# Kernel optimization log

Measured on AMD Instinct MI355X. Metric: run time of the kernel, lower is better.

Reference implementation:

```python
import jax, jax.numpy as jnp
import numpy as np

B, C, H, W = 8, 256, 128, 128
P = 7          # patch_size (odd)
N = 500        # n_infer (eval mode)
HIDDEN = C // 16  # reduction=16


def setup_inputs() -> dict:
    key = jax.random.key(0)
    ks = jax.random.split(key, 8)
    def s(k, shape, fan_in):
        return jax.random.normal(k, shape, jnp.float32) * (1.0 / np.sqrt(fan_in))
    return {
        "x_main": jax.random.normal(ks[0], (B, C, H, W), jnp.float32),
        "x_aux": jax.random.normal(ks[1], (B, C, H, W), jnp.float32),
        "scorer_w": s(ks[2], (C,), C),            # 1x1 conv C->1
        "scorer_b": s(ks[3], (1,), C),
        "fc1_w": s(ks[4], (3 * C, HIDDEN), 3 * C),
        "fc1_b": jnp.zeros((HIDDEN,), jnp.float32),
        "fc2_w": s(ks[5], (HIDDEN, C), HIDDEN),
        "fc2_b": jnp.zeros((C,), jnp.float32),
        "proj_w": s(ks[6], (C, C), C),
        "proj_b": jnp.zeros((C,), jnp.float32),
        "n": N,
    }


def _sample_patch_feats(feat, px, py):
    # feat: [C,H,W]; px,py: [n,p,p] pixel coords (align_corners=False convention).
    # Bilinear sample with zero padding, then pool 0.5*(mean+max) over the patch.
    c, h, w = feat.shape
    x0 = jnp.floor(px); y0 = jnp.floor(py)
    wx1 = px - x0; wy1 = py - y0
    def gather(yi, xi):
        valid = ((yi >= 0) & (yi < h) & (xi >= 0) & (xi < w)).astype(feat.dtype)
        yc = jnp.clip(yi, 0, h - 1).astype(jnp.int32)
        xc = jnp.clip(xi, 0, w - 1).astype(jnp.int32)
        return feat[:, yc, xc] * valid  # [C,n,p,p]
    patch = (gather(y0, x0) * ((1 - wy1) * (1 - wx1))
             + gather(y0, x0 + 1) * ((1 - wy1) * wx1)
             + gather(y0 + 1, x0) * (wy1 * (1 - wx1))
             + gather(y0 + 1, x0 + 1) * (wy1 * wx1))  # [C,n,p,p]
    v = 0.5 * (patch.mean(axis=(2, 3)) + patch.max(axis=(2, 3)))  # [C,n]
    return v.T  # [n,C]


def reference(x_main, x_aux, scorer_w, scorer_b, fc1_w, fc1_b, fc2_w, fc2_b, proj_w, proj_b, n):
    b, c, h, w = x_main.shape
    # saliency scores -> topk indices over flattened HW
    score = jax.nn.sigmoid(jnp.einsum('bchw,c->bhw', x_main, scorer_w) + scorer_b[0])
    score = score.reshape(b, h * w)
    _, idx = jax.lax.top_k(score, n)  # [b,n] int32
    idx_y = idx // w
    idx_x = idx - idx_y * w
    # build the (clamped) normalized grid exactly as the torch module does,
    # then convert to pixel coords: px = ((g+1)*W - 1)/2 (align_corners=False)
    r = P // 2
    d = jnp.arange(-r, r + 1, dtype=jnp.float32)
    yy, xx = jnp.meshgrid(d, d, indexing='ij')
    off_x = xx * (2.0 / w); off_y = yy * (2.0 / h)           # [p,p]
    cx = (idx_x.astype(jnp.float32) + 0.5) * (2.0 / w) - 1.0  # [b,n]
    cy = (idx_y.astype(jnp.float32) + 0.5) * (2.0 / h) - 1.0
    gx = jnp.clip(cx[:, :, None, None] + off_x, -1.0, 1.0)    # [b,n,p,p]
    gy = jnp.clip(cy[:, :, None, None] + off_y, -1.0, 1.0)
    px = ((gx + 1.0) * w - 1.0) * 0.5
    py = ((gy + 1.0) * h - 1.0) * 0.5
    sample = jax.vmap(_sample_patch_feats)
    v_main = sample(x_main, px, py)  # [b,n,C]
    v_aux = sample(x_aux, px, py)    # aux_in_proj is Identity (c_main==c_aux)
    # instance-level cross attention
    sim = jnp.einsum('bnc,bmc->bnm', v_main, v_aux) / jnp.sqrt(jnp.float32(c))
    attn = jax.nn.softmax(sim, axis=-1)
    v_hat = jnp.einsum('bnm,bmc->bnc', attn, v_aux)
    # gated fusion MLP
    z = jnp.concatenate([v_main, v_hat, v_main - v_hat], axis=-1)  # [b,n,3C]
    gate = jax.nn.sigmoid(jax.nn.relu(z @ fc1_w + fc1_b) @ fc2_w + fc2_b)
    v_fused = v_main + gate * (v_main - v_hat)
    v_inj = v_fused @ proj_w + proj_b  # [b,n,C]
    # scatter-add reinjection at the topk locations
    inject = jnp.zeros((b, h * w, c), x_main.dtype)
    inject = inject.at[jnp.arange(b)[:, None], idx].add(v_inj)
    inject = inject.reshape(b, h, w, c).transpose(0, 3, 1, 2)
    return x_main + inject
```

## Files before the change

### kernel.cpp

```cpp
#include <hip/hip_runtime.h>
#include <cstdint>
#include <cstddef>

#define HW    16384
#define CCH   256
#define WID   128
#define NB    8
#define NSEL  500
#define NPAD  512

__device__ __forceinline__ unsigned key_of(float f) {
  unsigned u = __float_as_uint(f);
  return (u & 0x80000000u) ? ~u : (u | 0x80000000u);
}

__global__ __launch_bounds__(256) void score_kernel(const float* __restrict__ x,
                                                    const float* __restrict__ w,
                                                    float* __restrict__ logits) {
  __shared__ float ws[CCH];
  int tid = threadIdx.x;
  ws[tid] = w[tid];
  __syncthreads();
  int pix = blockIdx.x * 256 + tid;
  int b = pix >> 14, p = pix & (HW - 1);
  const float* xp = x + ((size_t)b << 22) + p;
  float acc = 0.f;
#pragma unroll 16
  for (int c = 0; c < CCH; c++) acc += xp[(size_t)c * HW] * ws[c];
  logits[pix] = acc;
}

__global__ __launch_bounds__(1024) void topk_kernel(const float* __restrict__ logits,
                                                    int* __restrict__ idx_out,
                                                    int* __restrict__ map) {
  int b = blockIdx.x, tid = threadIdx.x;
  const float* lg = logits + (size_t)b * HW;
  __shared__ unsigned hist[256];
  __shared__ unsigned sscan[1024];
  __shared__ unsigned bc_prefix;
  __shared__ int bc_want;
  __shared__ int cnt;

  unsigned kreg[16];
#pragma unroll
  for (int j = 0; j < 4; j++) {
    float4 v = *(const float4*)&lg[tid * 16 + j * 4];
    kreg[4 * j + 0] = key_of(v.x);
    kreg[4 * j + 1] = key_of(v.y);
    kreg[4 * j + 2] = key_of(v.z);
    kreg[4 * j + 3] = key_of(v.w);
  }
  for (int p = tid; p < HW; p += 1024) map[(size_t)b * HW + p] = -1;

  unsigned prefix = 0;
  int want = NSEL;
  for (int shift = 24; shift >= 0; shift -= 8) {
    if (tid < 256) hist[tid] = 0;
    __syncthreads();
#pragma unroll
    for (int j = 0; j < 16; j++) {
      unsigned u = kreg[j];
      bool m = (shift == 24) || ((u >> (shift + 8)) == (prefix >> (shift + 8)));
      if (m) atomicAdd(&hist[(u >> shift) & 255u], 1u);
    }
    __syncthreads();
    unsigned h = (tid < 256) ? hist[tid] : 0u;
    if (tid < 256) sscan[tid] = h;
    __syncthreads();
    for (int o = 1; o < 256; o <<= 1) {
      unsigned v = (tid < 256 && tid + o < 256) ? sscan[tid + o] : 0u;
      __syncthreads();
      if (tid < 256) sscan[tid] += v;
      __syncthreads();
    }
    if (tid < 256) {
      unsigned above = sscan[tid] - h;
      if ((int)sscan[tid] >= want && (int)above < want) {
        bc_prefix = prefix | ((unsigned)tid << shift);
        bc_want = want - (int)above;
      }
    }
    __syncthreads();
    prefix = bc_prefix;
    want = bc_want;
    __syncthreads();
  }
  unsigned thr = prefix;

  int local = 0;
#pragma unroll
  for (int j = 0; j < 16; j++) local += (kreg[j] == thr) ? 1 : 0;
  sscan[tid] = (unsigned)local;
  if (tid == 0) cnt = 0;
  __syncthreads();
  for (int o = 1; o < 1024; o <<= 1) {
    unsigned v = (tid >= o) ? sscan[tid - o] : 0u;
    __syncthreads();
    sscan[tid] += v;
    __syncthreads();
  }
  int rank = (int)sscan[tid] - local;
#pragma unroll
  for (int j = 0; j < 16; j++) {
    unsigned u = kreg[j];
    bool take = (u > thr);
    if (u == thr) { if (rank < want) take = true; rank++; }
    if (take) {
      int s = atomicAdd(&cnt, 1);
      int p = tid * 16 + j;
      idx_out[b * NPAD + s] = p;
      map[(size_t)b * HW + p] = s;
    }
  }
}

__device__ __forceinline__ void patch_weights(int p, int* xc, int* yc, float* wx, float* wy) {
  int iy = p >> 7, ix = p & (WID - 1);
#pragma unroll
  for (int d = 0; d < 7; d++) {
    int t = ix + d - 3;
    bool in = (t >= 0) && (t < WID);
    xc[d] = in ? t : (t < 0 ? 0 : WID - 1);
    wx[d] = in ? 1.f : 0.5f;
    t = iy + d - 3;
    in = (t >= 0) && (t < WID);
    yc[d] = in ? t : (t < 0 ? 0 : WID - 1);
    wy[d] = in ? 1.f : 0.5f;
  }
}

__global__ __launch_bounds__(512) void gather_plane_kernel(const float* __restrict__ xm,
                                                           const float* __restrict__ xa,
                                                           const int* __restrict__ idx,
                                                           float* __restrict__ vmainT,
                                                           float* __restrict__ vauxT) {
  extern __shared__ float plane[];
  int c = blockIdx.x, b = blockIdx.y, z = blockIdx.z;
  int tid = threadIdx.x;
  const float* src = (z == 0 ? xm : xa) + ((size_t)(b * CCH + c)) * HW;
  float* dst = (z == 0 ? vmainT : vauxT) + (((size_t)(b * CCH + c)) << 9);
#pragma unroll
  for (int j = 0; j < 8; j++) {
    int p4 = tid + j * 512;
    *(float4*)&plane[p4 * 4] = *(const float4*)&src[p4 * 4];
  }
  __syncthreads();
  if (tid < NSEL) {
    int p = idx[b * NPAD + tid];
    float wx[7], wy[7];
    int xc[7], yc[7];
    patch_weights(p, xc, yc, wx, wy);
    float s = 0.f, mx = -INFINITY;
#pragma unroll
    for (int dy = 0; dy < 7; dy++) {
      int rb = yc[dy] * WID;
      float wyd = wy[dy];
#pragma unroll
      for (int dx = 0; dx < 7; dx++) {
        float v = plane[rb + xc[dx]] * (wyd * wx[dx]);
        s += v;
        mx = fmaxf(mx, v);
      }
    }
    dst[tid] = 0.5f * (s * (1.f / 49.f) + mx);
  }
}

template <int M, int N, int K, bool AT, bool BT, bool BSHARED, int EPI>
__global__ __launch_bounds__(256) void gemm_kernel(const float* __restrict__ A,
                                                   const float* __restrict__ B,
                                                   float* __restrict__ C,
                                                   const float* __restrict__ bias) {
  constexpr int BM = 64, BN = 64, BK = 16;
  __shared__ float As[BM][BK + 1];
  __shared__ float Bs[BK][BN + 1];
  int tid = threadIdx.x;
  int bx = blockIdx.x, by = blockIdx.y, b = blockIdx.z;
  const float* Ab = A + (size_t)b * M * K;
  const float* Bb = BSHARED ? B : (B + (size_t)b * ((size_t)K * N));
  int tx = tid & 15, ty = tid >> 4;
  float acc[4][4] = {};
  int ar = tid >> 2, ac4 = (tid & 3) * 4;
  int br = tid >> 4, bc4 = (tid & 15) * 4;

  for (int k0 = 0; k0 < K; k0 += BK) {
    if (!AT) {
      const float4 av = *(const float4*)&Ab[(size_t)(by * BM + ar) * K + k0 + ac4];
      As[ar][ac4 + 0] = av.x; As[ar][ac4 + 1] = av.y;
      As[ar][ac4 + 2] = av.z; As[ar][ac4 + 3] = av.w;
    } else {
      int kr = tid >> 4, mc = (tid & 15) * 4;
      const float4 av = *(const float4*)&Ab[(size_t)(k0 + kr) * M + by * BM + mc];
      As[mc + 0][kr] = av.x; As[mc + 1][kr] = av.y;
      As[mc + 2][kr] = av.z; As[mc + 3][kr] = av.w;
    }
    if (!BT) {
      const float4 bv = *(const float4*)&Bb[(size_t)(k0 + br) * N + bx * BN + bc4];
      Bs[br][bc4 + 0] = bv.x; Bs[br][bc4 + 1] = bv.y;
      Bs[br][bc4 + 2] = bv.z; Bs[br][bc4 + 3] = bv.w;
    } else {
      const float4 bv = *(const float4*)&Bb[(size_t)(bx * BN + ar) * K + k0 + ac4];
      Bs[ac4 + 0][ar] = bv.x; Bs[ac4 + 1][ar] = bv.y;
      Bs[ac4 + 2][ar] = bv.z; Bs[ac4 + 3][ar] = bv.w;
    }
    __syncthreads();
#pragma unroll
    for (int kk = 0; kk < BK; kk++) {
      float a[4], bb[4];
#pragma unroll
      for (int r = 0; r < 4; r++) a[r] = As[ty * 4 + r][kk];
#pragma unroll
      for (int s = 0; s < 4; s++) bb[s] = Bs[kk][tx * 4 + s];
#pragma unroll
      for (int r = 0; r < 4; r++)
#pragma unroll
        for (int s = 0; s < 4; s++) acc[r][s] += a[r] * bb[s];
    }
    __syncthreads();
  }
  if (EPI == 2) {
#pragma unroll
    for (int s = 0; s < 4; s++) {
      int col = bx * BN + tx * 4 + s;
      float bv = bias[col];
#pragma unroll
      for (int r = 0; r < 4; r++) {
        int row = by * BM + ty * 4 + r;
        C[((size_t)b * N + col) * M + row] = acc[r][s] + bv;
      }
    }
  } else {
    float scale = (EPI == 1) ? 0.0625f : 1.f;
#pragma unroll
    for (int r = 0; r < 4; r++) {
      int row = by * BM + ty * 4 + r;
#pragma unroll
      for (int s = 0; s < 4; s++) {
        int col = bx * BN + tx * 4 + s;
        C[((size_t)b * M + row) * N + col] = acc[r][s] * scale;
      }
    }
  }
}

__global__ __launch_bounds__(256) void softmax_kernel(float* __restrict__ sim) {
  int i = blockIdx.x, b = blockIdx.y, tid = threadIdx.x;
  float* row = sim + ((size_t)b * NPAD + i) * NPAD;
  float v0 = (tid < NSEL) ? row[tid] : -INFINITY;
  int j1 = tid + 256;
  float v1 = (j1 < NSEL) ? row[j1] : -INFINITY;
  float m = fmaxf(v0, v1);
  for (int o = 32; o; o >>= 1) m = fmaxf(m, __shfl_down(m, o));
  __shared__ float red[4];
  __shared__ float bm, bs;
  int wave = tid >> 6, lane = tid & 63;
  if (lane == 0) red[wave] = m;
  __syncthreads();
  if (tid == 0) bm = fmaxf(fmaxf(red[0], red[1]), fmaxf(red[2], red[3]));
  __syncthreads();
  m = bm;
  float e0 = (tid < NSEL) ? expf(v0 - m) : 0.f;
  float e1 = (j1 < NSEL) ? expf(v1 - m) : 0.f;
  float s = e0 + e1;
  for (int o = 32; o; o >>= 1) s += __shfl_down(s, o);
  if (lane == 0) red[wave] = s;
  __syncthreads();
  if (tid == 0) bs = 1.f / (red[0] + red[1] + red[2] + red[3]);
  __syncthreads();
  row[tid] = e0 * bs;
  row[j1] = e1 * bs;
}

__global__ __launch_bounds__(256) void mlp_kernel(const float* __restrict__ vmainT,
                                                  const float* __restrict__ vhat,
                                                  const float* __restrict__ fc1w,
                                                  const float* __restrict__ fc1b,
                                                  const float* __restrict__ fc2w,
                                                  const float* __restrict__ fc2b,
                                                  float* __restrict__ vfused) {
  int i = blockIdx.x, b = blockIdx.y, c = threadIdx.x;
  size_t base = ((size_t)b * NPAD + i) * CCH + c;
  float vm = vmainT[(((size_t)(b * CCH + c)) << 9) + i];
  float vh = vhat[base], vd = vm - vh;
  const float* w0 = fc1w + (size_t)c * 16;
  const float* w1 = fc1w + (size_t)(256 + c) * 16;
  const float* w2 = fc1w + (size_t)(512 + c) * 16;
  float ph[16];
#pragma unroll
  for (int k = 0; k < 16; k++) ph[k] = vm * w0[k] + vh * w1[k] + vd * w2[k];
#pragma unroll
  for (int o = 32; o; o >>= 1)
#pragma unroll
    for (int k = 0; k < 16; k++) ph[k] += __shfl_down(ph[k], o);
  __shared__ float red[4][16];
  __shared__ float hsh[16];
  int wave = c >> 6, lane = c & 63;
  if (lane == 0)
#pragma unroll
    for (int k = 0; k < 16; k++) red[wave][k] = ph[k];
  __syncthreads();
  if (c < 16) {
    float s = red[0][c] + red[1][c] + red[2][c] + red[3][c] + fc1b[c];
    hsh[c] = fmaxf(s, 0.f);
  }
  __syncthreads();
  float g = fc2b[c];
#pragma unroll
  for (int k = 0; k < 16; k++) g += hsh[k] * fc2w[k * 256 + c];
  g = 1.f / (1.f + expf(-g));
  vfused[base] = vm + g * vd;
}

__global__ __launch_bounds__(256) void final_kernel(const float* __restrict__ x,
                                                    const int* __restrict__ map,
                                                    const float* __restrict__ vinjT,
                                                    float* __restrict__ out) {
  int gid = blockIdx.x * 256 + threadIdx.x;
  int p4 = gid & 4095;
  int c = (gid >> 12) & 255;
  int b = gid >> 20;
  size_t xoff = (((size_t)(b * 256 + c)) << 14) + ((size_t)p4 << 2);
  float4 xv = *(const float4*)(x + xoff);
  const int4 mv = *(const int4*)(map + ((size_t)b << 14) + (p4 << 2));
  const float* vt = vinjT + ((size_t)(b * 256 + c) << 9);
  if (mv.x >= 0) xv.x += vt[mv.x];
  if (mv.y >= 0) xv.y += vt[mv.y];
  if (mv.z >= 0) xv.z += vt[mv.z];
  if (mv.w >= 0) xv.w += vt[mv.w];
  *(float4*)(out + xoff) = xv;
}

extern "C" void kernel_launch(void* const* d_in, const int* in_sizes, int n_in,
                              void* d_out, int out_size, void* d_ws, size_t ws_size,
                              hipStream_t stream) {
  const float* x_main   = (const float*)d_in[0];
  const float* x_aux    = (const float*)d_in[1];
  const float* scorer_w = (const float*)d_in[2];
  const float* fc1_w = (const float*)d_in[4];
  const float* fc1_b = (const float*)d_in[5];
  const float* fc2_w = (const float*)d_in[6];
  const float* fc2_b = (const float*)d_in[7];
  const float* proj_w = (const float*)d_in[8];
  const float* proj_b = (const float*)d_in[9];
  (void)in_sizes; (void)n_in; (void)out_size; (void)ws_size;

  float* ws = (float*)d_ws;
  float* logits = ws;
  int*   idx    = (int*)(ws + 131072);
  int*   map    = (int*)(ws + 135168);
  float* vmainT = ws + 266240;
  float* vauxT  = ws + 1314816;
  float* vhat   = ws + 2363392;
  float* vfused = ws + 3411968;
  float* sim    = ws + 4460544;
  float* vinjT  = vhat;
  float* out = (float*)d_out;

  score_kernel<<<512, 256, 0, stream>>>(x_main, scorer_w, logits);
  topk_kernel<<<NB, 1024, 0, stream>>>(logits, idx, map);
  gather_plane_kernel<<<dim3(CCH, NB, 2), 512, HW * sizeof(float), stream>>>(
      x_main, x_aux, idx, vmainT, vauxT);
  gemm_kernel<NPAD, NPAD, CCH, true, false, false, 1>
      <<<dim3(8, 8, NB), 256, 0, stream>>>(vmainT, vauxT, sim, nullptr);
  softmax_kernel<<<dim3(NPAD, NB), 256, 0, stream>>>(sim);
  gemm_kernel<NPAD, CCH, NPAD, false, true, false, 0>
      <<<dim3(4, 8, NB), 256, 0, stream>>>(sim, vauxT, vhat, nullptr);
  mlp_kernel<<<dim3(NPAD, NB), 256, 0, stream>>>(vmainT, vhat, fc1_w, fc1_b,
                                                 fc2_w, fc2_b, vfused);
  gemm_kernel<NPAD, CCH, CCH, false, false, true, 2>
      <<<dim3(4, 8, NB), 256, 0, stream>>>(vfused, proj_w, vinjT, proj_b);
  final_kernel<<<32768, 256, 0, stream>>>(x_main, map, vinjT, out);
}
```

Before: 540.8 us.

## Pipeline channel-plane loads in gather kernel and vectorize GEMM shared-memory reads

The gather kernel now handles 8 channels per block. It prefetches the next channel plane into registers while computing on the current plane in shared memory, and hoists index and weight setup so it runs once per block instead of once per channel. The patch reduction is also factored by rows. The GEMM stores its A tile k-major, so inner-loop reads become float4 shared-memory loads. The trade-off is fewer blocks in the gather (512 instead of 4096), higher register pressure from the 8 float4 prefetch, and it now writes zeros to the padded rows.

```diff
diff --git a/kernel.cpp b/kernel.cpp
--- a/kernel.cpp
+++ b/kernel.cpp
@@ -8,6 +8,7 @@
 #define NB    8
 #define NSEL  500
 #define NPAD  512
+#define CPG   8
 
 __device__ __forceinline__ unsigned key_of(float f) {
   unsigned u = __float_as_uint(f);
@@ -129,40 +130,64 @@
   }
 }
 
-__global__ __launch_bounds__(512) void gather_plane_kernel(const float* __restrict__ xm,
-                                                           const float* __restrict__ xa,
-                                                           const int* __restrict__ idx,
-                                                           float* __restrict__ vmainT,
-                                                           float* __restrict__ vauxT) {
+__global__ __launch_bounds__(512, 4) void gather_pipe_kernel(const float* __restrict__ xm,
+                                                             const float* __restrict__ xa,
+                                                             const int* __restrict__ idx,
+                                                             float* __restrict__ vmainT,
+                                                             float* __restrict__ vauxT) {
   extern __shared__ float plane[];
-  int c = blockIdx.x, b = blockIdx.y, z = blockIdx.z;
+  int g = blockIdx.x, b = blockIdx.y, z = blockIdx.z;
   int tid = threadIdx.x;
-  const float* src = (z == 0 ? xm : xa) + ((size_t)(b * CCH + c)) * HW;
-  float* dst = (z == 0 ? vmainT : vauxT) + (((size_t)(b * CCH + c)) << 9);
-#pragma unroll
-  for (int j = 0; j < 8; j++) {
-    int p4 = tid + j * 512;
-    *(float4*)&plane[p4 * 4] = *(const float4*)&src[p4 * 4];
-  }
-  __syncthreads();
-  if (tid < NSEL) {
-    int p = idx[b * NPAD + tid];
-    float wx[7], wy[7];
-    int xc[7], yc[7];
-    patch_weights(p, xc, yc, wx, wy);
-    float s = 0.f, mx = -INFINITY;
-#pragma unroll
-    for (int dy = 0; dy < 7; dy++) {
-      int rb = yc[dy] * WID;
-      float wyd = wy[dy];
-#pragma unroll
-      for (int dx = 0; dx < 7; dx++) {
-        float v = plane[rb + xc[dx]] * (wyd * wx[dx]);
-        s += v;
-        mx = fmaxf(mx, v);
+  int c0 = g * CPG;
+  const float* src = (z == 0 ? xm : xa) + ((size_t)(b * CCH + c0)) * HW;
+  float* dst = (z == 0 ? vmainT : vauxT) + (((size_t)(b * CCH + c0)) << 9);
+
+  int t500 = (tid < NSEL) ? tid : 0;
+  int p = idx[b * NPAD + t500];
+  float wx[7], wy[7];
+  int xc[7], yc[7], rb[7];
+  patch_weights(p, xc, yc, wx, wy);
+#pragma unroll
+  for (int d = 0; d < 7; d++) rb[d] = yc[d] * WID;
+
+  float4 r[8];
+#pragma unroll
+  for (int j = 0; j < 8; j++) r[j] = *(const float4*)&src[(size_t)(tid + j * 512) * 4];
+#pragma unroll
+  for (int j = 0; j < 8; j++) *(float4*)&plane[(tid + j * 512) * 4] = r[j];
+  __syncthreads();
+
+  for (int c = 0; c < CPG; c++) {
+    if (c + 1 < CPG) {
+      const float* s2 = src + (size_t)(c + 1) * HW;
+#pragma unroll
+      for (int j = 0; j < 8; j++) r[j] = *(const float4*)&s2[(size_t)(tid + j * 512) * 4];
+    }
+    if (tid < NSEL) {
+      float s = 0.f, mx = -INFINITY;
+#pragma unroll
+      for (int dy = 0; dy < 7; dy++) {
+        float rs = 0.f, rm = -INFINITY;
+        int rbb = rb[dy];
+#pragma unroll
+        for (int dx = 0; dx < 7; dx++) {
+          float v = plane[rbb + xc[dx]] * wx[dx];
+          rs += v;
+          rm = fmaxf(rm, v);
+        }
+        s += rs * wy[dy];
+        mx = fmaxf(mx, rm * wy[dy]);
       }
-    }
-    dst[tid] = 0.5f * (s * (1.f / 49.f) + mx);
+      dst[((size_t)c << 9) + tid] = 0.5f * (s * (1.f / 49.f) + mx);
+    } else {
+      dst[((size_t)c << 9) + tid] = 0.f;
+    }
+    if (c + 1 < CPG) {
+      __syncthreads();
+#pragma unroll
+      for (int j = 0; j < 8; j++) *(float4*)&plane[(tid + j * 512) * 4] = r[j];
+      __syncthreads();
+    }
   }
 }
 
@@ -172,49 +197,45 @@
                                                    float* __restrict__ C,
                                                    const float* __restrict__ bias) {
   constexpr int BM = 64, BN = 64, BK = 16;
-  __shared__ float As[BM][BK + 1];
-  __shared__ float Bs[BK][BN + 1];
+  __shared__ float As[BK][BM + 4];
+  __shared__ float Bs[BK][BN + 4];
   int tid = threadIdx.x;
   int bx = blockIdx.x, by = blockIdx.y, b = blockIdx.z;
   const float* Ab = A + (size_t)b * M * K;
   const float* Bb = BSHARED ? B : (B + (size_t)b * ((size_t)K * N));
   int tx = tid & 15, ty = tid >> 4;
   float acc[4][4] = {};
-  int ar = tid >> 2, ac4 = (tid & 3) * 4;
-  int br = tid >> 4, bc4 = (tid & 15) * 4;
 
   for (int k0 = 0; k0 < K; k0 += BK) {
     if (!AT) {
+      int ar = tid >> 2, ac4 = (tid & 3) * 4;
       const float4 av = *(const float4*)&Ab[(size_t)(by * BM + ar) * K + k0 + ac4];
-      As[ar][ac4 + 0] = av.x; As[ar][ac4 + 1] = av.y;
-      As[ar][ac4 + 2] = av.z; As[ar][ac4 + 3] = av.w;
+      As[ac4 + 0][ar] = av.x; As[ac4 + 1][ar] = av.y;
+      As[ac4 + 2][ar] = av.z; As[ac4 + 3][ar] = av.w;
     } else {
       int kr = tid >> 4, mc = (tid & 15) * 4;
-      const float4 av = *(const float4*)&Ab[(size_t)(k0 + kr) * M + by * BM + mc];
-      As[mc + 0][kr] = av.x; As[mc + 1][kr] = av.y;
-      As[mc + 2][kr] = av.z; As[mc + 3][kr] = av.w;
+      *(float4*)&As[kr][mc] = *(const float4*)&Ab[(size_t)(k0 + kr) * M + by * BM + mc];
     }
     if (!BT) {
-      const float4 bv = *(const float4*)&Bb[(size_t)(k0 + br) * N + bx * BN + bc4];
-      Bs[br][bc4 + 0] = bv.x; Bs[br][bc4 + 1] = bv.y;
-      Bs[br][bc4 + 2] = bv.z; Bs[br][bc4 + 3] = bv.w;
+      int br = tid >> 4, bc4 = (tid & 15) * 4;
+      *(float4*)&Bs[br][bc4] = *(const float4*)&Bb[(size_t)(k0 + br) * N + bx * BN + bc4];
     } else {
-      const float4 bv = *(const float4*)&Bb[(size_t)(bx * BN + ar) * K + k0 + ac4];
-      Bs[ac4 + 0][ar] = bv.x; Bs[ac4 + 1][ar] = bv.y;
-      Bs[ac4 + 2][ar] = bv.z; Bs[ac4 + 3][ar] = bv.w;
+      int nr = tid >> 2, kc4 = (tid & 3) * 4;
+      const float4 bv = *(const float4*)&Bb[(size_t)(bx * BN + nr) * K + k0 + kc4];
+      Bs[kc4 + 0][nr] = bv.x; Bs[kc4 + 1][nr] = bv.y;
+      Bs[kc4 + 2][nr] = bv.z; Bs[kc4 + 3][nr] = bv.w;
     }
     __syncthreads();
 #pragma unroll
     for (int kk = 0; kk < BK; kk++) {
-      float a[4], bb[4];
-#pragma unroll
-      for (int r = 0; r < 4; r++) a[r] = As[ty * 4 + r][kk];
-#pragma unroll
-      for (int s = 0; s < 4; s++) bb[s] = Bs[kk][tx * 4 + s];
-#pragma unroll
-      for (int r = 0; r < 4; r++)
-#pragma unroll
-        for (int s = 0; s < 4; s++) acc[r][s] += a[r] * bb[s];
+      const float4 a = *(const float4*)&As[kk][ty * 4];
+      const float4 bb = *(const float4*)&Bs[kk][tx * 4];
+      float av[4] = {a.x, a.y, a.z, a.w};
+      float bv[4] = {bb.x, bb.y, bb.z, bb.w};
+#pragma unroll
+      for (int rr = 0; rr < 4; rr++)
+#pragma unroll
+        for (int ss = 0; ss < 4; ss++) acc[rr][ss] += av[rr] * bv[ss];
     }
     __syncthreads();
   }
@@ -358,7 +379,7 @@
 
   score_kernel<<<512, 256, 0, stream>>>(x_main, scorer_w, logits);
   topk_kernel<<<NB, 1024, 0, stream>>>(logits, idx, map);
-  gather_plane_kernel<<<dim3(CCH, NB, 2), 512, HW * sizeof(float), stream>>>(
+  gather_pipe_kernel<<<dim3(CCH / CPG, NB, 2), 512, HW * sizeof(float), stream>>>(
       x_main, x_aux, idx, vmainT, vauxT);
   gemm_kernel<NPAD, NPAD, CCH, true, false, false, 1>
       <<<dim3(8, 8, NB), 256, 0, stream>>>(vmainT, vauxT, sim, nullptr);
```

Result: slower. 591.1 us (+9.3%).
